# Performance work log

Measured on AMD Instinct MI355X. Metric: run time of the kernel, lower is better.

## Reference

```python
import jax, jax.numpy as jnp
import numpy as np

N_CLUSTER = 1
SIZE, RATIO = 32, 0.1


def _lin_mat(n_in, n_out):
    # bilinear, align_corners=True interpolation matrix [n_out, n_in]
    src = np.arange(n_out) * (n_in - 1) / (n_out - 1)
    lo = np.floor(src).astype(np.int64)
    hi = np.minimum(lo + 1, n_in - 1)
    w = (src - lo).astype(np.float32)
    M = np.zeros((n_out, n_in), np.float32)
    M[np.arange(n_out), lo] += 1.0 - w
    M[np.arange(n_out), hi] += w
    return jnp.asarray(M)


def setup_inputs() -> dict:
    key = jax.random.key(0)
    ks = jax.random.split(key, 5)
    B, D, H, W, C = 16, 128, 128, 128, 6
    inp = {
        "assp": jax.random.normal(ks[0], (B, D, H, W), jnp.float32),
        "cls_w": jax.random.normal(ks[1], (C, D), jnp.float32) * 0.05,
        "cls_b": jnp.zeros((C,), jnp.float32),
        "key_w": jax.random.normal(ks[2], (128, D), jnp.float32) * 0.05,
        "key_b": jnp.zeros((128,), jnp.float32),
        "query_w": jax.random.normal(ks[3], (C, 128, D), jnp.float32) * 0.05,
        "query_b": jnp.zeros((C, 128), jnp.float32),
    }
    rng = np.random.default_rng(0)
    idx = rng.permutation(SIZE * SIZE)[: int(SIZE * SIZE * RATIO)]  # 102 unique pixels
    inp["px"] = jnp.asarray(idx // SIZE, jnp.int32)
    inp["py"] = jnp.asarray(idx % SIZE, jnp.int32)
    return inp


def reference(assp, cls_w, cls_b, key_w, key_b, query_w, query_b, px, py):
    B, D, H, W = assp.shape
    C = cls_w.shape[0]
    # pseudo labels (torch.no_grad)
    feats = jax.lax.stop_gradient(assp)
    pseudo = jnp.einsum('bdhw,cd->bchw', feats, cls_w) + cls_b[None, :, None, None]
    mask = jnp.argmax(pseudo, axis=1)                      # [B,H,W]
    onehot = jax.nn.one_hot(mask, C, dtype=assp.dtype)      # [B,H,W,C]
    counts = onehot.sum((1, 2))                             # [B,C]
    sums = jnp.einsum('bdhw,bhwc->bcd', assp, onehot)       # masked class sums
    protoC = sums / (counts[..., None] + 1e-5)              # [B,C,D]
    protoC = jnp.where(counts[..., None] > 0, protoC, 0.0)  # zero_prototype fallback
    protos12 = jnp.broadcast_to(protoC[:, :, None, :], (B, C, 2, D)).reshape(B, 2 * C, D)

    # DomainTrain: gather sampled pixels, L2 dist to 12 prototypes, argmin, scatter replace
    feat_px = assp[:, :, px, py]                            # [B,D,Np]
    diff = protos12[:, :, None, :] - feat_px.transpose(0, 2, 1)[:, None, :, :]  # [B,12,Np,D]
    dist = jnp.linalg.norm(diff, axis=-1)                   # [B,12,Np]
    closest = jnp.argmin(dist, axis=1)                      # [B,Np]
    repl = jnp.take_along_axis(protos12, closest[..., None], axis=1)  # [B,Np,D]
    assp = assp.at[:, :, px, py].set(repl.transpose(0, 2, 1))
    protos4 = protos12.reshape(B, C, 2, D)

    # key / query attention
    keymap = jnp.einsum('bdhw,kd->bkhw', assp, key_w) + key_b[None, :, None, None]
    q = jnp.einsum('bijd,ikd->bijk', protos4, query_w) + query_b[None, :, None, :]  # [B,C,2,128]
    sim = jnp.einsum('bijk,bkhw->bijhw', q, keymap).reshape(B, 2 * C, H, W)
    simw = jax.nn.softmax(sim / (2 * C) * N_CLUSTER, axis=1).mean(axis=1)  # [B,H,W]

    weighted = assp * simw[:, None]
    x = jnp.einsum('bdhw,cd->bchw', weighted, cls_w) + cls_b[None, :, None, None]
    My = _lin_mat(H, 4 * H)
    Mx = _lin_mat(W, 4 * W)
    xup = jnp.einsum('Hh,bchw,Ww->bcHW', My, x, Mx)
    return xup
```

## Files before the change

kernel.cpp:

```cpp
#include <hip/hip_runtime.h>

namespace {

constexpr int B  = 16;
constexpr int D  = 128;
constexpr int C  = 6;
constexpr int H  = 128;
constexpr int W  = 128;
constexpr int HWC = H * W;
constexpr int HO = 512, WO = 512;
constexpr int TILE = 64;
constexpr int TPB  = 8;

__global__ __launch_bounds__(256) void k_fused(const float* __restrict__ assp,
                                               const float* __restrict__ cls_w,
                                               const float* __restrict__ cls_b,
                                               float* __restrict__ sums,
                                               int* __restrict__ counts,
                                               float* __restrict__ x) {
  __shared__ float tile[D * TILE];
  __shared__ float red[4 * C * TILE];
  __shared__ float ws[C * D];
  __shared__ float bs[C];

  const int t  = threadIdx.x;
  const int b  = blockIdx.y;
  for (int i = t; i < C * D; i += 256) ws[i] = cls_w[i];
  if (t < C) bs[t] = cls_b[t];

  const int lane = t & 63;
  const int wv   = t >> 6;
  const int d2b  = t & 127;
  const int h2b  = t >> 7;
  const int d1   = t >> 5;
  const int px2  = (t & 31) * 2;

  float acc2b[C] = {0.f, 0.f, 0.f, 0.f, 0.f, 0.f};
  int   cnt_run  = 0;

  __syncthreads();

  for (int it = 0; it < TPB; ++it) {
    const int hw0 = (blockIdx.x * TPB + it) * TILE;
    const float* base = assp + ((size_t)b * D) * HWC + hw0;

    float2 v[16];
#pragma unroll
    for (int j = 0; j < 16; ++j) {
      int d = d1 + 8 * j;
      v[j] = *(const float2*)(base + (size_t)d * HWC + px2);
    }
#pragma unroll
    for (int j = 0; j < 16; ++j) {
      int d = d1 + 8 * j;
      *(float2*)&tile[d * TILE + (px2 ^ (d & 62))] = v[j];
    }
    __syncthreads();

    {
      float a[C] = {0.f, 0.f, 0.f, 0.f, 0.f, 0.f};
#pragma unroll
      for (int dd = 0; dd < 32; ++dd) {
        int d = wv * 32 + dd;
        float vv = tile[d * TILE + (lane ^ (d & 62))];
#pragma unroll
        for (int c = 0; c < C; ++c) a[c] += vv * ws[c * D + d];
      }
#pragma unroll
      for (int c = 0; c < C; ++c) red[(wv * C + c) * TILE + lane] = a[c];
    }
    __syncthreads();

    int cls;
    {
      float s[C];
#pragma unroll
      for (int c = 0; c < C; ++c)
        s[c] = red[(0 * C + c) * TILE + lane] + red[(1 * C + c) * TILE + lane]
             + red[(2 * C + c) * TILE + lane] + red[(3 * C + c) * TILE + lane];
      float bv = s[0] + bs[0]; cls = 0;
#pragma unroll
      for (int c = 1; c < C; ++c) {
        float pv = s[c] + bs[c];
        if (pv > bv) { bv = pv; cls = c; }
      }
      if (wv == 0) {
        const float inv12 = 1.0f / 12.0f;
        float* xb = x + ((size_t)b * C) * HWC + hw0 + lane;
#pragma unroll
        for (int c = 0; c < C; ++c) xb[(size_t)c * HWC] = s[c] * inv12 + bs[c];
#pragma unroll
        for (int c = 0; c < C; ++c) {
          unsigned long long m = __ballot(cls == c);
          if (lane == c) cnt_run += (int)__popcll(m);
        }
      }
    }

#pragma unroll
    for (int i = 0; i < 32; ++i) {
      int px = h2b * 32 + i;
      float vv = tile[d2b * TILE + (px ^ (d2b & 62))];
      int c = __shfl(cls, px, 64);
#pragma unroll
      for (int cc = 0; cc < C; ++cc) acc2b[cc] += (c == cc) ? vv : 0.f;
    }
    __syncthreads();
  }

  float* part = red;
  if (h2b == 1) {
#pragma unroll
    for (int c = 0; c < C; ++c) part[c * D + d2b] = acc2b[c];
  }
  __syncthreads();
  if (h2b == 0) {
#pragma unroll
    for (int c = 0; c < C; ++c) {
      float s = acc2b[c] + part[c * D + d2b];
      atomicAdd(&sums[((size_t)b * C + c) * D + d2b], s);
    }
  }
  if (wv == 0 && lane < C) atomicAdd(&counts[b * C + lane], cnt_run);
}

__global__ void k_patch(const float* __restrict__ assp,
                        const float* __restrict__ sums,
                        const int* __restrict__ counts,
                        const float* __restrict__ cls_w,
                        const float* __restrict__ cls_b,
                        const int* __restrict__ px,
                        const int* __restrict__ py,
                        int P,
                        float* __restrict__ x) {
  int bp = blockIdx.x;
  int b = bp / P, p = bp % P;
  int hw = px[p] * W + py[p];
  int lane = threadIdx.x;
  const float* fbase = assp + ((size_t)b * D) * HWC + hw;

  float f0 = fbase[(size_t)lane * HWC];
  float f1 = fbase[(size_t)(lane + 64) * HWC];

  float pv0[C], pv1[C], ds[C];
#pragma unroll
  for (int c = 0; c < C; ++c) {
    float cnt = (float)counts[b * C + c];
    float s0 = sums[((size_t)b * C + c) * D + lane];
    float s1 = sums[((size_t)b * C + c) * D + lane + 64];
    float q0 = (cnt > 0.f) ? s0 / (cnt + 1e-5f) : 0.f;
    float q1 = (cnt > 0.f) ? s1 / (cnt + 1e-5f) : 0.f;
    pv0[c] = q0; pv1[c] = q1;
    float e0 = q0 - f0, e1 = q1 - f1;
    float tt = e0 * e0 + e1 * e1;
#pragma unroll
    for (int off = 32; off >= 1; off >>= 1) tt += __shfl_xor(tt, off, 64);
    ds[c] = tt;
  }
  int best = 0; float bv = ds[0];
#pragma unroll
  for (int c = 1; c < C; ++c)
    if (ds[c] < bv) { bv = ds[c]; best = c; }

  float v0 = 0.f, v1 = 0.f;
#pragma unroll
  for (int c = 0; c < C; ++c) {
    if (best == c) { v0 = pv0[c]; v1 = pv1[c]; }
  }

  float myx = 0.f;
#pragma unroll
  for (int c = 0; c < C; ++c) {
    float tt = v0 * cls_w[c * D + lane] + v1 * cls_w[c * D + lane + 64];
#pragma unroll
    for (int off = 32; off >= 1; off >>= 1) tt += __shfl_xor(tt, off, 64);
    float val = tt * (1.0f / 12.0f) + cls_b[c];
    if (lane == c) myx = val;
  }
  if (lane < C) x[((size_t)b * C + lane) * HWC + hw] = myx;
}

__global__ void k_up(const float* __restrict__ x, float* __restrict__ out) {
  int t = blockIdx.x * 256 + threadIdx.x;
  int i = t * 4;
  int X  = i & (WO - 1);
  int Y  = (i >> 9) & (HO - 1);
  int bc = i >> 18;

  double sy = (double)(Y * (H - 1)) / (double)(HO - 1);
  int y0 = (int)sy;
  float wy = (float)(sy - (double)y0);
  int y1 = y0 + 1; if (y1 > H - 1) y1 = H - 1;

  const float* r0 = x + (size_t)bc * HWC + y0 * W;
  const float* r1 = x + (size_t)bc * HWC + y1 * W;

  float o[4];
#pragma unroll
  for (int j = 0; j < 4; ++j) {
    int Xj = X + j;
    double sx = (double)(Xj * (W - 1)) / (double)(WO - 1);
    int x0 = (int)sx;
    float wx = (float)(sx - (double)x0);
    int x1 = x0 + 1; if (x1 > W - 1) x1 = W - 1;

    float v00 = r0[x0], v01 = r0[x1], v10 = r1[x0], v11 = r1[x1];
    o[j] = (1.f - wy) * ((1.f - wx) * v00 + wx * v01)
         +        wy  * ((1.f - wx) * v10 + wx * v11);
  }
  float4 o4; o4.x = o[0]; o4.y = o[1]; o4.z = o[2]; o4.w = o[3];
  *(float4*)(out + i) = o4;
}

}

extern "C" void kernel_launch(void* const* d_in, const int* in_sizes, int n_in,
                              void* d_out, int out_size, void* d_ws, size_t ws_size,
                              hipStream_t stream) {
  const float* assp  = (const float*)d_in[0];
  const float* cls_w = (const float*)d_in[1];
  const float* cls_b = (const float*)d_in[2];
  const int*   px    = (const int*)d_in[7];
  const int*   py    = (const int*)d_in[8];
  const int    P     = in_sizes[7];

  char* ws = (char*)d_ws;
  float* sums   = (float*)ws;
  int*   counts = (int*)(ws + 49152);
  float* x      = (float*)(ws + 65536);

  float* out = (float*)d_out;

  hipMemsetAsync(ws, 0, 49152 + 384, stream);
  k_fused<<<dim3(HWC / (TILE * TPB), B), 256, 0, stream>>>(assp, cls_w, cls_b,
                                                           sums, counts, x);
  k_patch<<<B * P, 64, 0, stream>>>(assp, sums, counts, cls_w, cls_b, px, py, P, x);
  k_up<<<(B * C * HO * WO) / 1024, 256, 0, stream>>>(x, out);
}
```

Baseline: 277.1 us.

## Double-buffer fused tile loads and replace atomics with per-block partial sums

The fused classification kernel now prefetches the next tile's global loads into registers while the current tile is being processed. It uses two shared-memory buffers so one barrier per iteration can be dropped. Global atomicAdds and the workspace memset are replaced by per-block partial sums and counts, which the patch kernel reduces by looping over all 32 blocks per batch. This trades atomics and a memset launch for more register pressure, 64KB of LDS tile space, and redundant partial reduction in every patch block.

```diff
diff --git a/kernel.cpp b/kernel.cpp
--- a/kernel.cpp
+++ b/kernel.cpp
@@ -11,22 +11,21 @@
 constexpr int HO = 512, WO = 512;
 constexpr int TILE = 64;
 constexpr int TPB  = 8;
+constexpr int NBLK = HWC / (TILE * TPB);
 
 __global__ __launch_bounds__(256) void k_fused(const float* __restrict__ assp,
                                                const float* __restrict__ cls_w,
                                                const float* __restrict__ cls_b,
-                                               float* __restrict__ sums,
-                                               int* __restrict__ counts,
+                                               float* __restrict__ partials,
+                                               int* __restrict__ pcnt,
                                                float* __restrict__ x) {
-  __shared__ float tile[D * TILE];
+  __shared__ float buf[2][D * TILE];
   __shared__ float red[4 * C * TILE];
   __shared__ float ws[C * D];
   __shared__ float bs[C];
 
   const int t  = threadIdx.x;
   const int b  = blockIdx.y;
-  for (int i = t; i < C * D; i += 256) ws[i] = cls_w[i];
-  if (t < C) bs[t] = cls_b[t];
 
   const int lane = t & 63;
   const int wv   = t >> 6;
@@ -35,25 +34,38 @@
   const int d1   = t >> 5;
   const int px2  = (t & 31) * 2;
 
+  const float* base0 = assp + ((size_t)b * D) * HWC + blockIdx.x * (TILE * TPB);
+
+  float2 v[16];
+#pragma unroll
+  for (int j = 0; j < 16; ++j) {
+    int d = d1 + 8 * j;
+    v[j] = *(const float2*)(base0 + (size_t)d * HWC + px2);
+  }
+
+  for (int i = t; i < C * D; i += 256) ws[i] = cls_w[i];
+  if (t < C) bs[t] = cls_b[t];
+
   float acc2b[C] = {0.f, 0.f, 0.f, 0.f, 0.f, 0.f};
   int   cnt_run  = 0;
 
   __syncthreads();
 
   for (int it = 0; it < TPB; ++it) {
-    const int hw0 = (blockIdx.x * TPB + it) * TILE;
-    const float* base = assp + ((size_t)b * D) * HWC + hw0;
-
-    float2 v[16];
+    float* cur = buf[it & 1];
+
 #pragma unroll
     for (int j = 0; j < 16; ++j) {
       int d = d1 + 8 * j;
-      v[j] = *(const float2*)(base + (size_t)d * HWC + px2);
-    }
-#pragma unroll
-    for (int j = 0; j < 16; ++j) {
-      int d = d1 + 8 * j;
-      *(float2*)&tile[d * TILE + (px2 ^ (d & 62))] = v[j];
+      *(float2*)&cur[d * TILE + (px2 ^ (d & 62))] = v[j];
+    }
+    if (it + 1 < TPB) {
+      const float* basen = base0 + (it + 1) * TILE;
+#pragma unroll
+      for (int j = 0; j < 16; ++j) {
+        int d = d1 + 8 * j;
+        v[j] = *(const float2*)(basen + (size_t)d * HWC + px2);
+      }
     }
     __syncthreads();
 
@@ -62,7 +74,7 @@
 #pragma unroll
       for (int dd = 0; dd < 32; ++dd) {
         int d = wv * 32 + dd;
-        float vv = tile[d * TILE + (lane ^ (d & 62))];
+        float vv = cur[d * TILE + (lane ^ (d & 62))];
 #pragma unroll
         for (int c = 0; c < C; ++c) a[c] += vv * ws[c * D + d];
       }
@@ -86,6 +98,7 @@
       }
       if (wv == 0) {
         const float inv12 = 1.0f / 12.0f;
+        int hw0 = blockIdx.x * (TILE * TPB) + it * TILE;
         float* xb = x + ((size_t)b * C) * HWC + hw0 + lane;
 #pragma unroll
         for (int c = 0; c < C; ++c) xb[(size_t)c * HWC] = s[c] * inv12 + bs[c];
@@ -100,14 +113,14 @@
 #pragma unroll
     for (int i = 0; i < 32; ++i) {
       int px = h2b * 32 + i;
-      float vv = tile[d2b * TILE + (px ^ (d2b & 62))];
+      float vv = cur[d2b * TILE + (px ^ (d2b & 62))];
       int c = __shfl(cls, px, 64);
 #pragma unroll
       for (int cc = 0; cc < C; ++cc) acc2b[cc] += (c == cc) ? vv : 0.f;
     }
-    __syncthreads();
-  }
-
+  }
+
+  __syncthreads();
   float* part = red;
   if (h2b == 1) {
 #pragma unroll
@@ -115,18 +128,18 @@
   }
   __syncthreads();
   if (h2b == 0) {
-#pragma unroll
-    for (int c = 0; c < C; ++c) {
-      float s = acc2b[c] + part[c * D + d2b];
-      atomicAdd(&sums[((size_t)b * C + c) * D + d2b], s);
-    }
-  }
-  if (wv == 0 && lane < C) atomicAdd(&counts[b * C + lane], cnt_run);
+    float* ps = partials + ((size_t)(b * NBLK + blockIdx.x) * C) * D;
+#pragma unroll
+    for (int c = 0; c < C; ++c)
+      ps[c * D + d2b] = acc2b[c] + part[c * D + d2b];
+  }
+  if (wv == 0 && lane < C)
+    pcnt[(b * NBLK + blockIdx.x) * C + lane] = cnt_run;
 }
 
 __global__ void k_patch(const float* __restrict__ assp,
-                        const float* __restrict__ sums,
-                        const int* __restrict__ counts,
+                        const float* __restrict__ partials,
+                        const int* __restrict__ pcnt,
                         const float* __restrict__ cls_w,
                         const float* __restrict__ cls_b,
                         const int* __restrict__ px,
@@ -142,14 +155,24 @@
   float f0 = fbase[(size_t)lane * HWC];
   float f1 = fbase[(size_t)(lane + 64) * HWC];
 
+  float s0[C] = {0,0,0,0,0,0}, s1[C] = {0,0,0,0,0,0};
+  int   cn[C] = {0,0,0,0,0,0};
+  for (int blk = 0; blk < NBLK; ++blk) {
+    const float* pp = partials + ((size_t)(b * NBLK + blk) * C) * D;
+#pragma unroll
+    for (int c = 0; c < C; ++c) {
+      s0[c] += pp[c * D + lane];
+      s1[c] += pp[c * D + lane + 64];
+      cn[c] += pcnt[(b * NBLK + blk) * C + c];
+    }
+  }
+
   float pv0[C], pv1[C], ds[C];
 #pragma unroll
   for (int c = 0; c < C; ++c) {
-    float cnt = (float)counts[b * C + c];
-    float s0 = sums[((size_t)b * C + c) * D + lane];
-    float s1 = sums[((size_t)b * C + c) * D + lane + 64];
-    float q0 = (cnt > 0.f) ? s0 / (cnt + 1e-5f) : 0.f;
-    float q1 = (cnt > 0.f) ? s1 / (cnt + 1e-5f) : 0.f;
+    float cnt = (float)cn[c];
+    float q0 = (cnt > 0.f) ? s0[c] / (cnt + 1e-5f) : 0.f;
+    float q1 = (cnt > 0.f) ? s1[c] / (cnt + 1e-5f) : 0.f;
     pv0[c] = q0; pv1[c] = q1;
     float e0 = q0 - f0, e1 = q1 - f1;
     float tt = e0 * e0 + e1 * e1;
@@ -164,9 +187,8 @@
 
   float v0 = 0.f, v1 = 0.f;
 #pragma unroll
-  for (int c = 0; c < C; ++c) {
+  for (int c = 0; c < C; ++c)
     if (best == c) { v0 = pv0[c]; v1 = pv1[c]; }
-  }
 
   float myx = 0.f;
 #pragma unroll
@@ -225,15 +247,15 @@
   const int    P     = in_sizes[7];
 
   char* ws = (char*)d_ws;
-  float* sums   = (float*)ws;
-  int*   counts = (int*)(ws + 49152);
-  float* x      = (float*)(ws + 65536);
+  float* partials = (float*)ws;
+  int*   pcnt     = (int*)(ws + (size_t)B * NBLK * C * D * 4);
+  float* x        = (float*)(ws + (size_t)B * NBLK * C * D * 4 + B * NBLK * C * 4);
 
   float* out = (float*)d_out;
 
-  hipMemsetAsync(ws, 0, 49152 + 384, stream);
-  k_fused<<<dim3(HWC / (TILE * TPB), B), 256, 0, stream>>>(assp, cls_w, cls_b,
-                                                           sums, counts, x);
-  k_patch<<<B * P, 64, 0, stream>>>(assp, sums, counts, cls_w, cls_b, px, py, P, x);
+  k_fused<<<dim3(NBLK, B), 256, 0, stream>>>(assp, cls_w, cls_b,
+                                             partials, pcnt, x);
+  k_patch<<<B * P, 64, 0, stream>>>(assp, partials, pcnt, cls_w, cls_b,
+                                    px, py, P, x);
   k_up<<<(B * C * HO * WO) / 1024, 256, 0, stream>>>(x, out);
 }
```

Result: slower. 283.8 us (+2.4%).
